# Kernel optimization log

Hardware: AMD Instinct MI355X
Metric: run time of the kernel (lower is better)

The kernel has to match this reference:

```python
import jax, jax.numpy as jnp
import numpy as np

B, N, D = 8, 1024, 256   # batch, nodes, input_size
H, HO = 4, 64            # nhead, hidden_size/nhead
T = 5                    # number of edge types (len(edges))
NEG = -1e9
EPS = 1e-6


def setup_inputs() -> dict:
    key = jax.random.key(0)
    ks = jax.random.split(key, 6)
    nodes_embed = jax.random.normal(ks[0], (B, N, D), dtype=jnp.float32)
    node_adj = jax.random.randint(ks[1], (B, N, N), 0, T + 1)  # values 0..T, 0 = no edge
    # per-head projection W: xavier-ish scale
    W = jax.random.normal(ks[2], (H, D, HO), dtype=jnp.float32) * (1.0 / np.sqrt(D))
    # per-edge-type scoring linear (2*HO -> 1), split into src/dst halves
    a_src = jax.random.normal(ks[3], (H, T, HO), dtype=jnp.float32) * 0.1
    a_dst = jax.random.normal(ks[4], (H, T, HO), dtype=jnp.float32) * 0.1
    bias = jnp.zeros((H, HO), dtype=jnp.float32)
    ln_gamma = jnp.ones((H, HO), dtype=jnp.float32)
    ln_beta = jnp.zeros((H, HO), dtype=jnp.float32)
    return {
        'nodes_embed': nodes_embed,
        'node_adj': node_adj,
        'W': W,
        'a_src': a_src,
        'a_dst': a_dst,
        'bias': bias,
        'ln_gamma': ln_gamma,
        'ln_beta': ln_beta,
    }


def reference(nodes_embed, node_adj, W, a_src, a_dst, bias, ln_gamma, ln_beta):
    # h: [B, H, N, HO] -- all heads projected at once
    h = jnp.einsum('bnd,hde->bhne', nodes_embed, W)
    # The torch code concatenates [h_i, h_j] and applies a (2*HO -> 1) linear per
    # edge type; that equals e_src[t, i] + e_dst[t, j] with the linear weight split
    # into src/dst halves. Avoids materializing the O(N^2 * 2*HO) concat tensor.
    e_src = jnp.einsum('bhne,hte->bhtn', h, a_src)  # [B, H, T, N]
    e_dst = jnp.einsum('bhne,hte->bhtn', h, a_dst)  # [B, H, T, N]
    n_types = a_src.shape[1]
    weight = jnp.zeros(h.shape[:2] + (h.shape[2], h.shape[2]), dtype=h.dtype)  # [B,H,N,N]
    for t in range(n_types):  # small fixed loop over edge types
        mask = (node_adj == t + 1).astype(h.dtype)[:, None]  # [B,1,N,N]
        weight = weight + mask * (e_src[:, :, t, :, None] + e_dst[:, :, t, None, :])
    weight = jax.nn.leaky_relu(weight, negative_slope=0.01)
    weight = jnp.where(node_adj[:, None] == 0, NEG, weight)
    attention = jax.nn.softmax(weight, axis=-1)  # [B,H,N,N]
    dst = jnp.einsum('bhij,bhje->bhie', attention, h) + bias[None, :, None, :]
    out = jax.nn.relu(dst) + h  # dropout is identity (p=0)
    # per-head LayerNorm over HO, eps=1e-6 (biased variance, as torch)
    mu = out.mean(axis=-1, keepdims=True)
    var = out.var(axis=-1, keepdims=True)
    out = (out - mu) / jnp.sqrt(var + EPS) * ln_gamma[None, :, None, :] + ln_beta[None, :, None, :]
    # concat heads: [B,H,N,HO] -> [B,N,H*HO]
    b, hh, n, e = out.shape
    return out.transpose(0, 2, 1, 3).reshape(b, n, hh * e)
```

## Files before the change

### kernel.cpp

```cpp
#include <hip/hip_runtime.h>
#include <hip/hip_bf16.h>

#define Bn 8
#define Nn 1024
#define Dn 256
#define Hn 4
#define HOn 64
#define Tn 5
#define WTR 80
#define EDS 128

typedef short bf16x8 __attribute__((ext_vector_type(8)));
typedef float f32x4 __attribute__((ext_vector_type(4)));

__device__ __forceinline__ float b2f(unsigned short u) {
    unsigned x = ((unsigned)u) << 16;
    float f;
    __builtin_memcpy(&f, &x, 4);
    return f;
}
__device__ __forceinline__ unsigned bfr(float f) {
    unsigned u;
    __builtin_memcpy(&u, &f, 4);
    return (u + 0x7FFFu + ((u >> 16) & 1u)) >> 16;
}
__device__ __forceinline__ unsigned short f2b(float f) { return (unsigned short)bfr(f); }

__device__ __forceinline__ float fast_exp2(float x) {
#if __has_builtin(__builtin_amdgcn_exp2f)
    return __builtin_amdgcn_exp2f(x);
#else
    float r;
    asm("v_exp_f32 %0, %1" : "=v"(r) : "v"(x));
    return r;
#endif
}

__global__ __launch_bounds__(256) void k_signal(float* __restrict__ out, int n) {
    int i = blockIdx.x * 256 + threadIdx.x;
    if (i < n) out[i] = 100.0f;
}

__global__ __launch_bounds__(256) void k_transpose_w(const float* __restrict__ W,
                                                     const float* __restrict__ a_src,
                                                     const float* __restrict__ a_dst,
                                                     unsigned short* __restrict__ WP) {
    __shared__ float tile[64][65];
    __shared__ float arow_s[10][64];
    int h = blockIdx.x >> 2;
    int d0 = (blockIdx.x & 3) * 64;
    int c0 = threadIdx.x & 63;
    int r0 = threadIdx.x >> 6;
#pragma unroll
    for (int r = 0; r < 16; r++) {
        int d = r * 4 + r0;
        tile[d][c0] = W[((size_t)(h * Dn + d0 + d)) * HOn + c0];
    }
    __syncthreads();
    for (int t = r0; t < 2 * Tn; t += 4) {
        const float* av = (t < Tn) ? (a_src + (h * Tn + t) * HOn)
                                   : (a_dst + (h * Tn + t - Tn) * HOn);
        float s = 0.f;
#pragma unroll
        for (int e = 0; e < HOn; e++) s += tile[c0][e] * av[e];
        arow_s[t][c0] = s;
    }
    __syncthreads();
    int kcb = d0 >> 5;
#pragma unroll
    for (int it = 0; it < 3; it++) {
        int idx = threadIdx.x + it * 256;
        if (idx < 640) {
            int kcp = idx / 320;
            int rem = idx % 320;
            int et = rem >> 6;
            int ln = rem & 63;
            int quad = ln >> 4, l15 = ln & 15;
            int dl = kcp * 32 + quad * 8;
            int row = et * 16 + l15;
            union { bf16x8 v; unsigned short u[8]; } ov;
#pragma unroll
            for (int m = 0; m < 8; m++) {
                float x = (row < 64) ? tile[dl + m][row]
                                     : ((row < 74) ? arow_s[row - 64][dl + m] : 0.f);
                ov.u[m] = f2b(x);
            }
            *(bf16x8*)(WP + ((((size_t)h * 8 + kcb + kcp) * 5 + et) * 64 + ln) * 8) = ov.v;
        }
    }
}

__global__ __launch_bounds__(256) void k_proj(const float* __restrict__ X,
                                              const unsigned short* __restrict__ WP,
                                              const int* __restrict__ adj,
                                              unsigned short* __restrict__ hP,
                                              float* __restrict__ e_src,
                                              float* __restrict__ e_dst,
                                              unsigned* __restrict__ adjp) {
    __shared__ unsigned short xs[16][264];
    __shared__ unsigned short ptile[4][64][24];
    int tid = threadIdx.x;
    int w = tid >> 6;
    int lane = tid & 63;
    int quad = lane >> 4;
    int l15 = lane & 15;
    int b = blockIdx.x >> 6;
    int i0 = (blockIdx.x & 63) * 16;
    int h = w;
    int bh = b * Hn + h;

    {
        const int* arow = adj + ((size_t)(b * Nn + i0)) * Nn;
        unsigned* aout = adjp + ((size_t)(b * Nn + i0)) * Nn / 4;
#pragma unroll 4
        for (int k = 0; k < 16; k++) {
            int idx = tid + k * 256;
            int4 v = *(const int4*)(arow + (size_t)idx * 4);
            unsigned pk = (unsigned)(v.x & 0xFF) | ((unsigned)(v.y & 0xFF) << 8) |
                          ((unsigned)(v.z & 0xFF) << 16) | ((unsigned)(v.w & 0xFF) << 24);
            aout[idx] = pk;
        }
    }

#pragma unroll
    for (int it = 0; it < 4; it++) {
        int row = it * 4 + (tid >> 6);
        int col = (tid & 63) * 4;
        float4 v = *(const float4*)(X + ((size_t)(b * Nn + i0 + row)) * Dn + col);
        __hip_bfloat162 h0 = __float22bfloat162_rn(make_float2(v.x, v.y));
        __hip_bfloat162 h1 = __float22bfloat162_rn(make_float2(v.z, v.w));
        unsigned u0, u1;
        __builtin_memcpy(&u0, &h0, 4);
        __builtin_memcpy(&u1, &h1, 4);
        unsigned* dst = (unsigned*)&xs[row][col];
        dst[0] = u0;
        dst[1] = u1;
    }
    __syncthreads();

    bf16x8 Bx[8];
#pragma unroll
    for (int kc = 0; kc < 8; kc++)
        Bx[kc] = *(const bf16x8*)(&xs[l15][kc * 32 + quad * 8]);

    f32x4 acc[5] = {{0.f, 0.f, 0.f, 0.f}, {0.f, 0.f, 0.f, 0.f}, {0.f, 0.f, 0.f, 0.f},
                    {0.f, 0.f, 0.f, 0.f}, {0.f, 0.f, 0.f, 0.f}};
    const unsigned short* wbase = WP + (size_t)h * 8 * 5 * 64 * 8;
#pragma unroll
    for (int kc = 0; kc < 8; kc++) {
#pragma unroll
        for (int et = 0; et < 5; et++) {
            bf16x8 Aw = *(const bf16x8*)(wbase + (((size_t)kc * 5 + et) * 64 + lane) * 8);
            acc[et] = __builtin_amdgcn_mfma_f32_16x16x32_bf16(Aw, Bx[kc], acc[et], 0, 0, 0);
        }
    }

#pragma unroll
    for (int et = 0; et < 4; et++) {
#pragma unroll
        for (int reg = 0; reg < 4; reg++) {
            int e = et * 16 + quad * 4 + reg;
            ptile[w][e][l15] = f2b(acc[et][reg]);
        }
    }
    __builtin_amdgcn_s_waitcnt(0);
    {
        int jb = i0 >> 4;
        int e_lo = lane >> 5;
        int l15v = (lane >> 1) & 15;
        int q2 = lane & 1;
#pragma unroll
        for (int p = 0; p < 2; p++) {
            int et = 2 * p + e_lo;
            bf16x8 v = *(const bf16x8*)(&ptile[w][et * 16 + l15v][q2 * 8]);
            *(bf16x8*)(hP + (((size_t)bh * 64 + jb) * 4 + et) * 256 + l15v * 16 + q2 * 8) = v;
        }
    }
#pragma unroll
    for (int reg = 0; reg < 4; reg++) {
        int t = quad * 4 + reg;
        if (t < Tn)
            e_src[((size_t)bh * Tn + t) * Nn + i0 + l15] = acc[4][reg] * 1.4426950408889634f;
        else if (t < 2 * Tn)
            e_dst[((size_t)bh * Tn + (t - Tn)) * Nn + i0 + l15] = acc[4][reg] * 1.4426950408889634f;
    }
}

__global__ __launch_bounds__(512) void k_attn(const unsigned char* __restrict__ adjp,
                                              const float* __restrict__ e_src,
                                              const float* __restrict__ e_dst,
                                              const unsigned short* __restrict__ hP,
                                              const float* __restrict__ bias,
                                              const float* __restrict__ gamma,
                                              const float* __restrict__ beta,
                                              float* __restrict__ out) {
    __shared__ __align__(16) unsigned short p_lds[8][16][136];
    __shared__ float es2[4][16][8];
    __shared__ float l_lds[8][16];
    __shared__ __align__(16) float ed_lds[8][6 * EDS];
    float* macc = (float*)&p_lds[4][0][0];

    int tid = threadIdx.x;
    int w = tid >> 6;
    int lane = tid & 63;
    int quad = lane >> 4;
    int l15 = lane & 15;
    int hh = w & 3;
    int half = w >> 2;
    int b = blockIdx.x >> 6;
    int i0 = (blockIdx.x & 63) * 16;
    int bh = b * Hn + hh;
    int J0 = half * 512;

    const unsigned char* adj_base = adjp + ((size_t)(b * Nn + i0)) * Nn + J0;
    const float* edst = e_dst + (size_t)bh * Tn * Nn + J0;
    const unsigned short* hPb = hP + (size_t)bh * 64 * 1024;

    int c0 = 2 * lane;
    float* edw = &ed_lds[w][0];

    f32x4 acc[4] = {{0.f, 0.f, 0.f, 0.f}, {0.f, 0.f, 0.f, 0.f},
                    {0.f, 0.f, 0.f, 0.f}, {0.f, 0.f, 0.f, 0.f}};
    f32x4 accl = {0.f, 0.f, 0.f, 0.f};
    bf16x8 ONES;
    {
        short o = (short)0x3F80;
        ONES = (bf16x8){o, o, o, o, o, o, o, o};
    }

    edw[c0] = -3e38f;
    edw[c0 + 1] = -3e38f;

    unsigned adjC[16], adjN[16];
#pragma unroll
    for (int r = 0; r < 16; r++)
        adjC[r] = *(const unsigned short*)(adj_base + (size_t)r * Nn + c0);
    float2 edr[Tn];
#pragma unroll
    for (int t = 0; t < Tn; t++) edr[t] = *(const float2*)(edst + t * Nn + c0);

    if (w < 4) {
        const float* esrc = e_src + (size_t)bh * Tn * Nn;
#pragma unroll
        for (int idx = lane; idx < 96; idx += 64) {
            int t = idx >> 4, row = idx & 15;
            es2[w][row][t] = t ? esrc[(t - 1) * Nn + i0 + row] : 0.f;
        }
    }
    __syncthreads();

#define P1ROW(ROW, AV)                                                          \
    {                                                                           \
        int a0 = (int)((AV) & 0xFFu);                                           \
        int a1 = (int)((AV) >> 8);                                              \
        float e0 = es2[hh][ROW][a0];                                            \
        float e1 = es2[hh][ROW][a1];                                            \
        float d0 = edw[a0 * EDS + c0];                                          \
        float d1 = edw[a1 * EDS + c0 + 1];                                      \
        float x0 = e0 + d0; x0 = fmaxf(x0, 0.01f * x0);                         \
        float x1 = e1 + d1; x1 = fmaxf(x1, 0.01f * x1);                         \
        float p0 = fast_exp2(x0);                                               \
        float p1 = fast_exp2(x1);                                               \
        __hip_bfloat162 pp = __float22bfloat162_rn(make_float2(p0, p1));        \
        unsigned pu; __builtin_memcpy(&pu, &pp, 4);                             \
        *(unsigned*)(&p_lds[w][ROW][2 * lane]) = pu;                            \
    }

#pragma unroll 1
    for (int c = 0; c < 4; c++) {
        int jc = c * 128;
#pragma unroll
        for (int t = 0; t < Tn; t++) {
            int wi = (t + 1) * EDS + c0;
            edw[wi] = edr[t].x;
            edw[wi + 1] = edr[t].y;
        }
        if (c < 3) {
#pragma unroll
            for (int r = 0; r < 16; r++)
                adjN[r] = *(const unsigned short*)(adj_base + (size_t)r * Nn + jc + 128 + c0);
#pragma unroll
            for (int t = 0; t < Tn; t++)
                edr[t] = *(const float2*)(edst + t * Nn + jc + 128 + c0);
        }
#pragma unroll
        for (int r = 0; r < 16; r++) P1ROW(r, adjC[r]);
#pragma unroll
        for (int k = 0; k < 4; k++) {
            bf16x8 Afr = *(const bf16x8*)(&p_lds[w][l15][k * 32 + quad * 8]);
            accl = __builtin_amdgcn_mfma_f32_16x16x32_bf16(Afr, ONES, accl, 0, 0, 0);
            int jb = ((J0 + jc + k * 32) >> 4) + (quad >> 1);
#pragma unroll
            for (int et = 0; et < 4; et++) {
                bf16x8 Bf = *(const bf16x8*)(hPb + ((size_t)jb * 4 + et) * 256 +
                                             l15 * 16 + (quad & 1) * 8);
                acc[et] = __builtin_amdgcn_mfma_f32_16x16x32_bf16(Afr, Bf, acc[et], 0, 0, 0);
            }
        }
        if (c < 3) {
#pragma unroll
            for (int r = 0; r < 16; r++) adjC[r] = adjN[r];
        }
    }
#undef P1ROW

    if (l15 == 0) {
#pragma unroll
        for (int reg = 0; reg < 4; reg++) l_lds[w][quad * 4 + reg] = accl[reg];
    }
    __syncthreads();
    if (w >= 4) {
#pragma unroll
        for (int et = 0; et < 4; et++)
#pragma unroll
            for (int reg = 0; reg < 4; reg++)
                macc[((hh * 16) + quad * 4 + reg) * 64 + et * 16 + l15] = acc[et][reg];
    }
    __syncthreads();
    if (w >= 4) return;

    float bv[4], gv[4], bev[4];
#pragma unroll
    for (int et = 0; et < 4; et++) {
        int e = et * 16 + l15;
        bv[et] = bias[hh * HOn + e];
        gv[et] = gamma[hh * HOn + e];
        bev[et] = beta[hh * HOn + e];
    }
    int jbe = i0 >> 4;
#pragma unroll
    for (int reg = 0; reg < 4; reg++) {
        int r = quad * 4 + reg;
        int i = i0 + r;
        float lw = l_lds[w][r] + l_lds[w + 4][r];
        float linv = 1.f / fmaxf(lw, 1e-30f);
        float dv[4];
        float s = 0.f, ss = 0.f;
        int q2 = r >> 3, m = r & 7;
#pragma unroll
        for (int et = 0; et < 4; et++) {
            int e = et * 16 + l15;
            float v = (acc[et][reg] + macc[((hh * 16) + r) * 64 + e]) * linv + bv[et];
            v = (v > 0.f) ? v : 0.f;
            v += b2f(hPb[((size_t)jbe * 4 + et) * 256 + l15 * 16 + q2 * 8 + m]);
            dv[et] = v;
            s += v;
            ss += v * v;
        }
#pragma unroll
        for (int off = 8; off; off >>= 1) {
            s += __shfl_xor(s, off);
            ss += __shfl_xor(ss, off);
        }
        float mean = s * (1.f / 64.f);
        float var = ss * (1.f / 64.f) - mean * mean;
        float rstd = rsqrtf(var + 1e-6f);
#pragma unroll
        for (int et = 0; et < 4; et++) {
            int e = et * 16 + l15;
            float o = (dv[et] - mean) * rstd * gv[et] + bev[et];
            out[((size_t)(b * Nn + i)) * (Hn * HOn) + hh * HOn + e] = o;
        }
    }
}

extern "C" void kernel_launch(void* const* d_in, const int* in_sizes, int n_in,
                              void* d_out, int out_size, void* d_ws, size_t ws_size,
                              hipStream_t stream) {
    const float* X = (const float*)d_in[0];
    const int* adj = (const int*)d_in[1];
    const float* W = (const float*)d_in[2];
    const float* a_src = (const float*)d_in[3];
    const float* a_dst = (const float*)d_in[4];
    const float* bias = (const float*)d_in[5];
    const float* gamma = (const float*)d_in[6];
    const float* beta = (const float*)d_in[7];
    float* out = (float*)d_out;

    char* ws = (char*)d_ws;
    size_t off = 0;
    unsigned short* hP = (unsigned short*)(ws + off);  off += (size_t)Bn * Hn * Nn * HOn * 2;
    unsigned short* WP = (unsigned short*)(ws + off);  off += (size_t)Hn * WTR * Dn * 2;
    float* e_src = (float*)(ws + off);                 off += (size_t)Bn * Hn * Tn * Nn * 4;
    float* e_dst = (float*)(ws + off);                 off += (size_t)Bn * Hn * Tn * Nn * 4;
    unsigned char* adjp = (unsigned char*)(ws + off);  off += (size_t)Bn * Nn * Nn;

    if (ws_size < off) {
        k_signal<<<(out_size + 255) / 256, 256, 0, stream>>>(out, out_size);
        return;
    }

    k_transpose_w<<<Hn * (Dn / 64), 256, 0, stream>>>(W, a_src, a_dst, WP);
    k_proj<<<Bn * (Nn / 16), 256, 0, stream>>>(X, WP, adj, hP, e_src, e_dst, (unsigned*)adjp);
    k_attn<<<Bn * (Nn / 16), 512, 0, stream>>>(adjp, e_src, e_dst, hP, bias, gamma, beta, out);
}
```

Measured before the change: 124.0 us.

## Compute attention probabilities directly in MFMA A-fragment layout, dropping LDS staging

Each lane now computes its probability values in the register layout the MFMA A operand expects: row l15 and eight consecutive columns per k-step. The results are packed into bf16x8 fragments without going through the p_lds shared-memory buffer. Adjacency is loaded as 8-byte chunks per row instead of 2-byte strided loads across 16 rows. The e_src/e_dst LDS strides are padded (EDS 132, es2 width 9) to reduce bank conflicts, macc gets its own buffer, and one __syncthreads is removed. The gather from ed_lds now uses per-lane type-dependent addresses that may still conflict on banks.

Measured after the change: 125.9 us. No clear change (+1.5%).

```diff
diff --git a/kernel.cpp b/kernel.cpp
--- a/kernel.cpp
+++ b/kernel.cpp
@@ -8,7 +8,7 @@
 #define HOn 64
 #define Tn 5
 #define WTR 80
-#define EDS 128
+#define EDS 132
 
 typedef short bf16x8 __attribute__((ext_vector_type(8)));
 typedef float f32x4 __attribute__((ext_vector_type(4)));
@@ -194,11 +194,10 @@
                                               const float* __restrict__ gamma,
                                               const float* __restrict__ beta,
                                               float* __restrict__ out) {
-    __shared__ __align__(16) unsigned short p_lds[8][16][136];
-    __shared__ float es2[4][16][8];
+    __shared__ float es2[4][16][9];
     __shared__ float l_lds[8][16];
     __shared__ __align__(16) float ed_lds[8][6 * EDS];
-    float* macc = (float*)&p_lds[4][0][0];
+    __shared__ float macc[4][16][64];
 
     int tid = threadIdx.x;
     int w = tid >> 6;
@@ -212,12 +211,14 @@
     int bh = b * Hn + hh;
     int J0 = half * 512;
 
-    const unsigned char* adj_base = adjp + ((size_t)(b * Nn + i0)) * Nn + J0;
+    const unsigned char* adj_row = adjp + ((size_t)(b * Nn + i0 + l15)) * Nn + J0;
     const float* edst = e_dst + (size_t)bh * Tn * Nn + J0;
     const unsigned short* hPb = hP + (size_t)bh * 64 * 1024;
 
     int c0 = 2 * lane;
+    int q8 = quad * 8;
     float* edw = &ed_lds[w][0];
+    const float* esb = &es2[hh][l15][0];
 
     f32x4 acc[4] = {{0.f, 0.f, 0.f, 0.f}, {0.f, 0.f, 0.f, 0.f},
                     {0.f, 0.f, 0.f, 0.f}, {0.f, 0.f, 0.f, 0.f}};
@@ -231,10 +232,10 @@
     edw[c0] = -3e38f;
     edw[c0 + 1] = -3e38f;
 
-    unsigned adjC[16], adjN[16];
-#pragma unroll
-    for (int r = 0; r < 16; r++)
-        adjC[r] = *(const unsigned short*)(adj_base + (size_t)r * Nn + c0);
+    unsigned long long adjQ[4], adjN[4];
+#pragma unroll
+    for (int k = 0; k < 4; k++)
+        adjQ[k] = *(const unsigned long long*)(adj_row + k * 32 + q8);
     float2 edr[Tn];
 #pragma unroll
     for (int t = 0; t < Tn; t++) edr[t] = *(const float2*)(edst + t * Nn + c0);
@@ -248,23 +249,6 @@
         }
     }
     __syncthreads();
-
-#define P1ROW(ROW, AV)                                                          \
-    {                                                                           \
-        int a0 = (int)((AV) & 0xFFu);                                           \
-        int a1 = (int)((AV) >> 8);                                              \
-        float e0 = es2[hh][ROW][a0];                                            \
-        float e1 = es2[hh][ROW][a1];                                            \
-        float d0 = edw[a0 * EDS + c0];                                          \
-        float d1 = edw[a1 * EDS + c0 + 1];                                      \
-        float x0 = e0 + d0; x0 = fmaxf(x0, 0.01f * x0);                         \
-        float x1 = e1 + d1; x1 = fmaxf(x1, 0.01f * x1);                         \
-        float p0 = fast_exp2(x0);                                               \
-        float p1 = fast_exp2(x1);                                               \
-        __hip_bfloat162 pp = __float22bfloat162_rn(make_float2(p0, p1));        \
-        unsigned pu; __builtin_memcpy(&pu, &pp, 4);                             \
-        *(unsigned*)(&p_lds[w][ROW][2 * lane]) = pu;                            \
-    }
 
 #pragma unroll 1
     for (int c = 0; c < 4; c++) {
@@ -277,44 +261,60 @@
         }
         if (c < 3) {
 #pragma unroll
-            for (int r = 0; r < 16; r++)
-                adjN[r] = *(const unsigned short*)(adj_base + (size_t)r * Nn + jc + 128 + c0);
+            for (int k = 0; k < 4; k++)
+                adjN[k] = *(const unsigned long long*)(adj_row + jc + 128 + k * 32 + q8);
 #pragma unroll
             for (int t = 0; t < Tn; t++)
                 edr[t] = *(const float2*)(edst + t * Nn + jc + 128 + c0);
         }
-#pragma unroll
-        for (int r = 0; r < 16; r++) P1ROW(r, adjC[r]);
+        bf16x8 pa[4];
 #pragma unroll
         for (int k = 0; k < 4; k++) {
-            bf16x8 Afr = *(const bf16x8*)(&p_lds[w][l15][k * 32 + quad * 8]);
-            accl = __builtin_amdgcn_mfma_f32_16x16x32_bf16(Afr, ONES, accl, 0, 0, 0);
+            float pv[8];
+#pragma unroll
+            for (int m = 0; m < 8; m++) {
+                int a = (int)((adjQ[k] >> (8 * m)) & 0xFFull);
+                float e0 = esb[a];
+                float d0 = edw[a * EDS + k * 32 + q8 + m];
+                float x = e0 + d0;
+                x = fmaxf(x, 0.01f * x);
+                pv[m] = fast_exp2(x);
+            }
+            union { bf16x8 v; unsigned u[4]; } pk;
+#pragma unroll
+            for (int j = 0; j < 4; j++) {
+                __hip_bfloat162 pp = __float22bfloat162_rn(make_float2(pv[2 * j], pv[2 * j + 1]));
+                __builtin_memcpy(&pk.u[j], &pp, 4);
+            }
+            pa[k] = pk.v;
+        }
+#pragma unroll
+        for (int k = 0; k < 4; k++) {
+            accl = __builtin_amdgcn_mfma_f32_16x16x32_bf16(pa[k], ONES, accl, 0, 0, 0);
             int jb = ((J0 + jc + k * 32) >> 4) + (quad >> 1);
 #pragma unroll
             for (int et = 0; et < 4; et++) {
                 bf16x8 Bf = *(const bf16x8*)(hPb + ((size_t)jb * 4 + et) * 256 +
                                              l15 * 16 + (quad & 1) * 8);
-                acc[et] = __builtin_amdgcn_mfma_f32_16x16x32_bf16(Afr, Bf, acc[et], 0, 0, 0);
+                acc[et] = __builtin_amdgcn_mfma_f32_16x16x32_bf16(pa[k], Bf, acc[et], 0, 0, 0);
             }
         }
         if (c < 3) {
 #pragma unroll
-            for (int r = 0; r < 16; r++) adjC[r] = adjN[r];
-        }
-    }
-#undef P1ROW
+            for (int k = 0; k < 4; k++) adjQ[k] = adjN[k];
+        }
+    }
 
     if (l15 == 0) {
 #pragma unroll
         for (int reg = 0; reg < 4; reg++) l_lds[w][quad * 4 + reg] = accl[reg];
     }
-    __syncthreads();
     if (w >= 4) {
 #pragma unroll
         for (int et = 0; et < 4; et++)
 #pragma unroll
             for (int reg = 0; reg < 4; reg++)
-                macc[((hh * 16) + quad * 4 + reg) * 64 + et * 16 + l15] = acc[et][reg];
+                macc[hh][quad * 4 + reg][et * 16 + l15] = acc[et][reg];
     }
     __syncthreads();
     if (w >= 4) return;
@@ -340,7 +340,7 @@
 #pragma unroll
         for (int et = 0; et < 4; et++) {
             int e = et * 16 + l15;
-            float v = (acc[et][reg] + macc[((hh * 16) + r) * 64 + e]) * linv + bv[et];
+            float v = (acc[et][reg] + macc[hh][r][e]) * linv + bv[et];
             v = (v > 0.f) ? v : 0.f;
             v += b2f(hPb[((size_t)jbe * 4 + et) * 256 + l15 * 16 + q2 * 8 + m]);
             dv[et] = v;
```
